# Performance work log

Measured on AMD Instinct MI355X. Metric: run time of the kernel, lower is better.

Reference implementation:

```python
import jax, jax.numpy as jnp
import numpy as np

V = 20000   # input_size (POI vocab)
U = 10000   # user_count
H = 128     # hidden_size
B = 64      # user_len (batch)
S = 200     # seq_len
LAM_T = 0.01
LAM_S = 100.0
DAY = 86400.0


def setup_inputs() -> dict:
    key = jax.random.key(0)
    ks = jax.random.split(key, 12)
    sc = 1.0 / np.sqrt(H)
    return {
        "poi_inputs": jax.random.randint(ks[0], (B, S), 0, V),
        "lengths": jnp.full((B,), S, dtype=jnp.int32),  # full sequences -> pack/pad is identity
        "timestamp_inputs": jnp.sort(jax.random.uniform(ks[1], (B, S), minval=0.0, maxval=DAY), axis=1),
        "location_inputs": jax.random.normal(ks[2], (B, S, 2)) * 0.1,
        "active_user": jax.random.randint(ks[3], (B,), 0, U),
        "emb_W": jax.random.normal(ks[4], (V, H)),      # nn.Embedding default N(0,1)
        "user_W": jax.random.normal(ks[5], (U, H)),
        "W_ih": jax.random.uniform(ks[6], (H, H), minval=-sc, maxval=sc),
        "W_hh": jax.random.uniform(ks[7], (H, H), minval=-sc, maxval=sc),
        "b_ih": jax.random.uniform(ks[8], (H,), minval=-sc, maxval=sc),
        "b_hh": jax.random.uniform(ks[9], (H,), minval=-sc, maxval=sc),
        "fc_W": jax.random.uniform(ks[10], (V, 2 * H), minval=-sc, maxval=sc),  # torch Linear [out,in]
        "fc_b": jax.random.uniform(ks[11], (V,), minval=-sc, maxval=sc),
    }


def _safe_norm(d):
    # norm over last axis with zero (not nan) gradient at d == 0
    d2 = jnp.sum(d * d, axis=-1)
    pos = d2 > 0
    return jnp.where(pos, jnp.sqrt(jnp.where(pos, d2, 1.0)), 0.0)


def reference(poi_inputs, lengths, timestamp_inputs, location_inputs, active_user,
              emb_W, user_W, W_ih, W_hh, b_ih, b_hh, fc_W, fc_b):
    t, s = timestamp_inputs, location_inputs
    x_emb = emb_W[poi_inputs]                       # [B,S,H]

    # vanilla tanh RNN (torch nn.RNN, batch_first) via scan over time
    def step(h, xt):
        h = jnp.tanh(xt @ W_ih.T + b_ih + h @ W_hh.T + b_hh)
        return h, h
    h0 = jnp.zeros((x_emb.shape[0], W_hh.shape[0]), x_emb.dtype)
    _, out = jax.lax.scan(step, h0, jnp.swapaxes(x_emb, 0, 1))
    out = jnp.swapaxes(out, 0, 1)                   # [B,S,H]

    # vectorized spatio-temporal decay attention (original O(S^2) python loop)
    dt = jnp.maximum(t[:, :, None] - t[:, None, :], 0.0)          # [B,S,S] clamp_min(0)
    ds = _safe_norm(s[:, :, None, :] - s[:, None, :, :])          # [B,S,S]
    a_j = ((jnp.cos(dt * (2.0 * jnp.pi / DAY)) + 1.0) * 0.5) * jnp.exp(-dt * LAM_T)
    b_j = jnp.exp(-ds * LAM_S)
    causal = jnp.tril(jnp.ones((t.shape[1], t.shape[1]), bool))   # j <= i
    w = jnp.where(causal, a_j * b_j + 1e-10, 0.0)                 # [B,S,S]
    sum_w = jnp.maximum(jnp.sum(w, axis=-1), 1e-10)               # [B,S]
    out_w = jnp.einsum('bij,bjh->bih', w, out) / sum_w[..., None] # [B,S,H]

    p_u = jnp.broadcast_to(user_W[active_user][:, None, :], out_w.shape)
    out_pu = jnp.concatenate([out_w, p_u], axis=-1)               # [B,S,2H]
    y = jax.nn.softmax(out_pu @ fc_W.T + fc_b, axis=-1)           # [B,S,V]
    return y, out_pu
```

## Files before the change

### kernel.cpp

```cpp
#include <hip/hip_runtime.h>
#include <hip/hip_bf16.h>
#include <stdint.h>

#define B_   64
#define S_   200
#define H_   128
#define V_   20000
#define M_   12800
#define NPAD 20224
#define NBN  158
#define NBM  100
#define NWG2 15800

#define WS_A      0u
#define WS_FCW    3276800u
#define WS_U      8454144u
#define WS_RSUM   13631488u
#define WS_WTIH   13682688u

#define XP_OFF    0
#define HOUT_OFF  2000000
#define PART_OFF  4000000
#define OUTPU_OFF 256000000ll

typedef __attribute__((ext_vector_type(8))) __bf16 bf16x8;
typedef __attribute__((ext_vector_type(4))) float  f32x4;

__device__ __forceinline__ void gll16(const void* g, void* l) {
  __builtin_amdgcn_global_load_lds(
      (const __attribute__((address_space(1))) void*)g,
      (__attribute__((address_space(3))) void*)l, 16, 0, 0);
}

__global__ __launch_bounds__(256)
void prep_w1(const float* __restrict__ fcw, __hip_bfloat16* __restrict__ w1) {
  int t = threadIdx.x;
  int row = blockIdx.x * 2 + (t >> 7);
  int col = t & 127;
  float v = (row < V_) ? fcw[(long)row * 256 + col] : 0.f;
  w1[(long)row * 128 + col] = __float2bfloat16(v);
}

__global__ __launch_bounds__(128)
void prep_wt(const float* __restrict__ w_ih, float* __restrict__ wt) {
  int bid = blockIdx.x, t = threadIdx.x;
  wt[bid * 128 + t] = w_ih[t * 128 + bid];
}

__global__ __launch_bounds__(256)
void user_k(const int* __restrict__ auser, const float* __restrict__ userW,
            const float* __restrict__ fcW, const float* __restrict__ fcb,
            float* __restrict__ U) {
  __shared__ float uw[8][128];
  int t = threadIdx.x;
  int c = blockIdx.x * 256 + t;
  int b0 = blockIdx.y * 8;
  for (int i = t; i < 8 * 128; i += 256) {
    int bb = i >> 7, kk = i & 127;
    uw[bb][kk] = userW[(long)auser[b0 + bb] * 128 + kk];
  }
  __syncthreads();
  float acc[8];
#pragma unroll
  for (int bb = 0; bb < 8; ++bb) acc[bb] = 0.f;
  if (c < V_) {
    const float* w2 = fcW + (long)c * 256 + 128;
#pragma unroll 4
    for (int k = 0; k < 128; k += 4) {
      float4 wv = *(const float4*)(w2 + k);
#pragma unroll
      for (int bb = 0; bb < 8; ++bb) {
        acc[bb] = fmaf(wv.x, uw[bb][k], acc[bb]);
        acc[bb] = fmaf(wv.y, uw[bb][k + 1], acc[bb]);
        acc[bb] = fmaf(wv.z, uw[bb][k + 2], acc[bb]);
        acc[bb] = fmaf(wv.w, uw[bb][k + 3], acc[bb]);
      }
    }
    float base = fcb[c];
#pragma unroll
    for (int bb = 0; bb < 8; ++bb)
      U[(long)(b0 + bb) * NPAD + c] = base + acc[bb];
  } else {
#pragma unroll
    for (int bb = 0; bb < 8; ++bb)
      U[(long)(b0 + bb) * NPAD + c] = -1e30f;
  }
}

__global__ __launch_bounds__(128)
void xproj_k(const int* __restrict__ poi, const float* __restrict__ emb,
             const float* __restrict__ wt_ih, const float* __restrict__ b_ih,
             const float* __restrict__ b_hh, float* __restrict__ xp) {
  __shared__ float xs[128];
  int m = blockIdx.x, j = threadIdx.x;
  xs[j] = emb[(long)poi[m] * 128 + j];
  __syncthreads();
  float acc = b_ih[j] + b_hh[j];
#pragma unroll 8
  for (int k = 0; k < 128; ++k) acc = fmaf(xs[k], wt_ih[k * 128 + j], acc);
  xp[(long)m * 128 + j] = acc;
}

__global__ __launch_bounds__(128)
void rnn_k(const float* __restrict__ xp, const float* __restrict__ w_hh,
           float* __restrict__ hout) {
  int b = blockIdx.x, j = threadIdx.x;
  float w[128];
#pragma unroll
  for (int k = 0; k < 128; ++k) w[k] = w_hh[j * 128 + k];
  __shared__ float hs[2][128];
  hs[0][j] = 0.f;
  __syncthreads();
  int cur = 0;
  for (int t = 0; t < S_; ++t) {
    float x0 = xp[((long)b * S_ + t) * 128 + j];
    const float* hp = hs[cur];
    float a0 = 0.f, a1 = 0.f, a2 = 0.f, a3 = 0.f;
#pragma unroll
    for (int k = 0; k < 32; ++k) {
      a0 = fmaf(hp[k],      w[k],      a0);
      a1 = fmaf(hp[k + 32], w[k + 32], a1);
      a2 = fmaf(hp[k + 64], w[k + 64], a2);
      a3 = fmaf(hp[k + 96], w[k + 96], a3);
    }
    float hn = tanhf(x0 + ((a0 + a1) + (a2 + a3)));
    hs[cur ^ 1][j] = hn;
    hout[((long)b * S_ + t) * 128 + j] = hn;
    cur ^= 1;
    __syncthreads();
  }
}

__global__ __launch_bounds__(128)
void attn_k(const float* __restrict__ ts, const float* __restrict__ loc,
            const float* __restrict__ hout, const int* __restrict__ auser,
            const float* __restrict__ userW, float* __restrict__ outpu,
            __hip_bfloat16* __restrict__ Abf) {
  int i = blockIdx.x, b = blockIdx.y, h = threadIdx.x;
  __shared__ float wl[128];
  const float OMEGA = 7.27220521664304e-05f;
  float ti = ts[b * S_ + i];
  float lx = loc[(b * S_ + i) * 2 + 0];
  float ly = loc[(b * S_ + i) * 2 + 1];
  float acc = 0.f, sw = 0.f;
  for (int jc = 0; jc <= i; jc += 128) {
    int j = jc + h;
    float wj = 0.f;
    if (j <= i) {
      float dt = fmaxf(ti - ts[b * S_ + j], 0.f);
      float a = (cosf(dt * OMEGA) + 1.f) * 0.5f * expf(-dt * 0.01f);
      float dx = lx - loc[(b * S_ + j) * 2 + 0];
      float dy = ly - loc[(b * S_ + j) * 2 + 1];
      float dn = sqrtf(dx * dx + dy * dy);
      wj = a * expf(-dn * 100.f) + 1e-10f;
    }
    __syncthreads();
    wl[h] = wj;
    __syncthreads();
    int lim = min(128, i - jc + 1);
    const float* hb = hout + ((long)b * S_ + jc) * 128 + h;
    for (int jj = 0; jj < lim; ++jj) {
      float wv = wl[jj];
      acc = fmaf(wv, hb[(long)jj * 128], acc);
      sw += wv;
    }
  }
  float ow = acc / fmaxf(sw, 1e-10f);
  long m = (long)b * S_ + i;
  float pu = userW[(long)auser[b] * 128 + h];
  outpu[m * 256 + h]       = ow;
  outpu[m * 256 + 128 + h] = pu;
  Abf[m * 128 + h]         = __float2bfloat16(ow);
}

template <int PASS>
__global__ __launch_bounds__(256)
void gemm_fc(const __hip_bfloat16* __restrict__ A,
             const __hip_bfloat16* __restrict__ Bw,
             const float* __restrict__ Ut,
             const float* __restrict__ rowsum,
             float* __restrict__ part,
             float* __restrict__ y) {
  __shared__ __align__(16) char smem[32768];
  __shared__ float rsum2[2][128];
  char* AsB = smem;
  char* BsB = smem + 8192;
  float* lbuf = (float*)smem;

  const int tid  = threadIdx.x;
  const int lane = tid & 63;
  const int wid  = tid >> 6;
  const int wr = wid >> 1, wc = wid & 1;
  const int g = lane >> 4, lr = lane & 15;

  const int orig = blockIdx.x;
  const int nid = (orig & 7) * (NWG2 / 8) + (orig >> 3);
  const int bn = nid / NBM, bm = nid % NBM;
  const long brow = (long)bm * 128, bcol = (long)bn * 128;

  f32x4 acc[4][4];
#pragma unroll
  for (int mi = 0; mi < 4; ++mi)
#pragma unroll
    for (int ni = 0; ni < 4; ++ni) acc[mi][ni] = (f32x4)(0.f);

  const char* Ab = (const char*)A + brow * 256;
  const char* Bb = (const char*)Bw + bcol * 256;
  const int c0 = tid, c1 = tid + 256;
  const int r0 = c0 >> 2, o0 = (c0 & 3) * 16;
  const int r1 = c1 >> 2, o1 = (c1 & 3) * 16;

  for (int kk = 0; kk < 4; ++kk) {
    __syncthreads();
    const int kb = kk * 64;
    gll16(Ab + (long)r0 * 256 + kb + o0, AsB + c0 * 16);
    gll16(Ab + (long)r1 * 256 + kb + o1, AsB + c1 * 16);
    gll16(Bb + (long)r0 * 256 + kb + o0, BsB + c0 * 16);
    gll16(Bb + (long)r1 * 256 + kb + o1, BsB + c1 * 16);
    __syncthreads();
    bf16x8 af[4], bfr[4];
#pragma unroll
    for (int mi = 0; mi < 4; ++mi)
      af[mi] = *(const bf16x8*)(AsB + (wr * 64 + mi * 16 + lr) * 64 + g * 16);
#pragma unroll
    for (int ni = 0; ni < 4; ++ni)
      bfr[ni] = *(const bf16x8*)(BsB + (wc * 64 + ni * 16 + lr) * 64 + g * 16);
#pragma unroll
    for (int mi = 0; mi < 4; ++mi)
#pragma unroll
      for (int ni = 0; ni < 4; ++ni)
        acc[mi][ni] = __builtin_amdgcn_mfma_f32_16x16x32_bf16(af[mi], bfr[ni], acc[mi][ni], 0, 0, 0);
  }

  if (PASS == 0) {
#pragma unroll
    for (int mi = 0; mi < 4; ++mi) {
#pragma unroll
      for (int r = 0; r < 4; ++r) {
        long row = brow + wr * 64 + mi * 16 + g * 4 + r;
        const float* urow = Ut + (long)(row / S_) * NPAD + bcol;
        float s = 0.f;
#pragma unroll
        for (int ni = 0; ni < 4; ++ni) {
          float u = urow[wc * 64 + ni * 16 + lr];
          s += __expf(acc[mi][ni][r] + u);
        }
#pragma unroll
        for (int off = 1; off < 16; off <<= 1) s += __shfl_xor(s, off);
        if (lr == 0) rsum2[wc][wr * 64 + mi * 16 + g * 4 + r] = s;
      }
    }
    __syncthreads();
    if (tid < 128)
      part[(long)bn * M_ + brow + tid] = rsum2[0][tid] + rsum2[1][tid];
  } else {
    if (bcol >= V_) return;
    const bool full = (bcol + 128 <= V_);
#pragma unroll
    for (int half = 0; half < 2; ++half) {
      __syncthreads();
      if (wr == half) {
#pragma unroll
        for (int mi = 0; mi < 4; ++mi) {
#pragma unroll
          for (int r = 0; r < 4; ++r) {
            int lrow = mi * 16 + g * 4 + r;
            long row = brow + half * 64 + lrow;
            const float* urow = Ut + (long)(row / S_) * NPAD + bcol;
            float inv = 1.0f / rowsum[row];
#pragma unroll
            for (int ni = 0; ni < 4; ++ni) {
              int lcol = wc * 64 + ni * 16 + lr;
              lbuf[lrow * 128 + lcol] = __expf(acc[mi][ni][r] + urow[lcol]) * inv;
            }
          }
        }
      }
      __syncthreads();
      if (full) {
#pragma unroll
        for (int it = 0; it < 8; ++it) {
          int idx = it * 256 + tid;
          int lrow = idx >> 5, c4 = idx & 31;
          long row = brow + half * 64 + lrow;
          *(float4*)(y + row * (long)V_ + bcol + c4 * 4) = ((const float4*)lbuf)[idx];
        }
      } else {
#pragma unroll
        for (int it = 0; it < 8; ++it) {
          int idx = it * 256 + tid;
          int lrow = idx >> 5, c4 = idx & 31;
          long row = brow + half * 64 + lrow;
#pragma unroll
          for (int e = 0; e < 4; ++e) {
            int col = (int)bcol + c4 * 4 + e;
            if (col < V_) y[row * (long)V_ + col] = lbuf[lrow * 128 + c4 * 4 + e];
          }
        }
      }
    }
  }
}

__global__ void reduce_rows(const float* __restrict__ part, float* __restrict__ rowsum) {
  int m = blockIdx.x * 256 + threadIdx.x;
  if (m < M_) {
    float s = 0.f;
    for (int bn = 0; bn < NBN; ++bn) s += part[(long)bn * M_ + m];
    rowsum[m] = fmaxf(s, 1e-30f);
  }
}

extern "C" void kernel_launch(void* const* d_in, const int* in_sizes, int n_in,
                              void* d_out, int out_size, void* d_ws, size_t ws_size,
                              hipStream_t stream) {
  const int*   poi   = (const int*)d_in[0];
  const float* ts    = (const float*)d_in[2];
  const float* loc   = (const float*)d_in[3];
  const int*   auser = (const int*)d_in[4];
  const float* embW  = (const float*)d_in[5];
  const float* userW = (const float*)d_in[6];
  const float* w_ih  = (const float*)d_in[7];
  const float* w_hh  = (const float*)d_in[8];
  const float* b_ih  = (const float*)d_in[9];
  const float* b_hh  = (const float*)d_in[10];
  const float* fcW   = (const float*)d_in[11];
  const float* fcb   = (const float*)d_in[12];

  float* out = (float*)d_out;
  char*  ws  = (char*)d_ws;
  __hip_bfloat16* Abf    = (__hip_bfloat16*)(ws + WS_A);
  __hip_bfloat16* w1b    = (__hip_bfloat16*)(ws + WS_FCW);
  float*          Ut     = (float*)(ws + WS_U);
  float*          rowsum = (float*)(ws + WS_RSUM);
  float*          wt_ih  = (float*)(ws + WS_WTIH);

  float* xp    = out + XP_OFF;
  float* hout  = out + HOUT_OFF;
  float* part  = out + PART_OFF;
  float* outpu = out + OUTPU_OFF;

  prep_w1<<<dim3(NPAD / 2), dim3(256), 0, stream>>>(fcW, w1b);
  prep_wt<<<dim3(128), dim3(128), 0, stream>>>(w_ih, wt_ih);
  user_k<<<dim3(NPAD / 256, 8), dim3(256), 0, stream>>>(auser, userW, fcW, fcb, Ut);
  xproj_k<<<dim3(M_), dim3(128), 0, stream>>>(poi, embW, wt_ih, b_ih, b_hh, xp);
  rnn_k<<<dim3(B_), dim3(128), 0, stream>>>(xp, w_hh, hout);
  attn_k<<<dim3(S_, B_), dim3(128), 0, stream>>>(ts, loc, hout, auser, userW, outpu, Abf);
  gemm_fc<0><<<dim3(NWG2), dim3(256), 0, stream>>>(Abf, w1b, Ut, nullptr, part, nullptr);
  reduce_rows<<<dim3(50), dim3(256), 0, stream>>>(part, rowsum);
  gemm_fc<1><<<dim3(NWG2), dim3(256), 0, stream>>>(Abf, w1b, Ut, rowsum, nullptr, out);
}
```

Baseline: 828.2 us.

## Enlarge FC GEMM tiles to 256x256 with full-K LDS staging and XOR swizzle

The two-pass FC softmax GEMM now uses 256x256 output tiles with 512 threads. The whole K=128 slice of A and B is loaded into 128KB of LDS in one go, with an XOR swizzle to avoid bank conflicts, and the per-K synchronisations are dropped. The XCD block remap now handles a block count that is not a multiple of 8. The aim is to cut redundant global reads of A and fcW and to reduce barrier overhead. In exchange, LDS use and register pressure rise (acc grows to 8x4), which limits occupancy to one block per CU.

```diff
diff --git a/kernel.cpp b/kernel.cpp
--- a/kernel.cpp
+++ b/kernel.cpp
@@ -8,9 +8,9 @@
 #define V_   20000
 #define M_   12800
 #define NPAD 20224
-#define NBN  158
-#define NBM  100
-#define NWG2 15800
+#define NBN  79
+#define NBM  50
+#define NWG  3950
 
 #define WS_A      0u
 #define WS_FCW    3276800u
@@ -174,59 +174,69 @@
 }
 
 template <int PASS>
-__global__ __launch_bounds__(256)
+__global__ __launch_bounds__(512)
 void gemm_fc(const __hip_bfloat16* __restrict__ A,
              const __hip_bfloat16* __restrict__ Bw,
              const float* __restrict__ Ut,
              const float* __restrict__ rowsum,
              float* __restrict__ part,
              float* __restrict__ y) {
-  __shared__ __align__(16) char smem[32768];
-  __shared__ float rsum2[2][128];
+  __shared__ __align__(16) char smem[131072];
+  __shared__ float rsum4[4][256];
   char* AsB = smem;
-  char* BsB = smem + 8192;
+  char* BsB = smem + 65536;
   float* lbuf = (float*)smem;
 
   const int tid  = threadIdx.x;
   const int lane = tid & 63;
   const int wid  = tid >> 6;
-  const int wr = wid >> 1, wc = wid & 1;
+  const int wr = wid >> 2, wc = wid & 3;
   const int g = lane >> 4, lr = lane & 15;
 
   const int orig = blockIdx.x;
-  const int nid = (orig & 7) * (NWG2 / 8) + (orig >> 3);
+  const int qq = NWG >> 3, rr = NWG & 7;
+  const int xcd = orig & 7, lix = orig >> 3;
+  const int nid = (xcd < rr ? xcd * (qq + 1) : rr * (qq + 1) + (xcd - rr) * qq) + lix;
   const int bn = nid / NBM, bm = nid % NBM;
-  const long brow = (long)bm * 128, bcol = (long)bn * 128;
-
-  f32x4 acc[4][4];
-#pragma unroll
-  for (int mi = 0; mi < 4; ++mi)
-#pragma unroll
-    for (int ni = 0; ni < 4; ++ni) acc[mi][ni] = (f32x4)(0.f);
+  const long brow = (long)bm * 256, bcol = (long)bn * 256;
 
   const char* Ab = (const char*)A + brow * 256;
   const char* Bb = (const char*)Bw + bcol * 256;
-  const int c0 = tid, c1 = tid + 256;
-  const int r0 = c0 >> 2, o0 = (c0 & 3) * 16;
-  const int r1 = c1 >> 2, o1 = (c1 & 3) * 16;
-
+
+#pragma unroll
+  for (int i = 0; i < 8; ++i) {
+    int ci = i * 512 + tid;
+    int row = ci >> 4;
+    int w = (ci & 15) ^ (row & 7);
+    long src = (long)row * 256 + (long)w * 16;
+    gll16(Ab + src, AsB + (long)ci * 16);
+    gll16(Bb + src, BsB + (long)ci * 16);
+  }
+  __syncthreads();
+
+  f32x4 acc[8][4];
+#pragma unroll
+  for (int mi = 0; mi < 8; ++mi)
+#pragma unroll
+    for (int ni = 0; ni < 4; ++ni) acc[mi][ni] = (f32x4)(0.f);
+
+#pragma unroll
   for (int kk = 0; kk < 4; ++kk) {
-    __syncthreads();
-    const int kb = kk * 64;
-    gll16(Ab + (long)r0 * 256 + kb + o0, AsB + c0 * 16);
-    gll16(Ab + (long)r1 * 256 + kb + o1, AsB + c1 * 16);
-    gll16(Bb + (long)r0 * 256 + kb + o0, BsB + c0 * 16);
-    gll16(Bb + (long)r1 * 256 + kb + o1, BsB + c1 * 16);
-    __syncthreads();
-    bf16x8 af[4], bfr[4];
-#pragma unroll
-    for (int mi = 0; mi < 4; ++mi)
-      af[mi] = *(const bf16x8*)(AsB + (wr * 64 + mi * 16 + lr) * 64 + g * 16);
-#pragma unroll
-    for (int ni = 0; ni < 4; ++ni)
-      bfr[ni] = *(const bf16x8*)(BsB + (wc * 64 + ni * 16 + lr) * 64 + g * 16);
-#pragma unroll
-    for (int mi = 0; mi < 4; ++mi)
+    bf16x8 af[8], bfr[4];
+#pragma unroll
+    for (int mi = 0; mi < 8; ++mi) {
+      int row = wr * 128 + mi * 16 + lr;
+      int w = ((kk << 2) | g) ^ (row & 7);
+      af[mi] = *(const bf16x8*)(AsB + row * 256 + w * 16);
+    }
+#pragma unroll
+    for (int ni = 0; ni < 4; ++ni) {
+      int row = wc * 64 + ni * 16 + lr;
+      int w = ((kk << 2) | g) ^ (row & 7);
+      bfr[ni] = *(const bf16x8*)(BsB + row * 256 + w * 16);
+    }
+#pragma unroll
+    for (int mi = 0; mi < 8; ++mi)
 #pragma unroll
       for (int ni = 0; ni < 4; ++ni)
         acc[mi][ni] = __builtin_amdgcn_mfma_f32_16x16x32_bf16(af[mi], bfr[ni], acc[mi][ni], 0, 0, 0);
@@ -234,10 +244,10 @@
 
   if (PASS == 0) {
 #pragma unroll
-    for (int mi = 0; mi < 4; ++mi) {
+    for (int mi = 0; mi < 8; ++mi) {
 #pragma unroll
       for (int r = 0; r < 4; ++r) {
-        long row = brow + wr * 64 + mi * 16 + g * 4 + r;
+        long row = brow + wr * 128 + mi * 16 + g * 4 + r;
         const float* urow = Ut + (long)(row / S_) * NPAD + bcol;
         float s = 0.f;
 #pragma unroll
@@ -247,31 +257,31 @@
         }
 #pragma unroll
         for (int off = 1; off < 16; off <<= 1) s += __shfl_xor(s, off);
-        if (lr == 0) rsum2[wc][wr * 64 + mi * 16 + g * 4 + r] = s;
+        if (lr == 0) rsum4[wc][wr * 128 + mi * 16 + g * 4 + r] = s;
       }
     }
     __syncthreads();
-    if (tid < 128)
-      part[(long)bn * M_ + brow + tid] = rsum2[0][tid] + rsum2[1][tid];
+    if (tid < 256)
+      part[(long)bn * M_ + brow + tid] =
+          rsum4[0][tid] + rsum4[1][tid] + rsum4[2][tid] + rsum4[3][tid];
   } else {
-    if (bcol >= V_) return;
-    const bool full = (bcol + 128 <= V_);
+    const bool full = (bcol + 256 <= V_);
 #pragma unroll
     for (int half = 0; half < 2; ++half) {
       __syncthreads();
       if (wr == half) {
 #pragma unroll
-        for (int mi = 0; mi < 4; ++mi) {
+        for (int mi = 0; mi < 8; ++mi) {
 #pragma unroll
           for (int r = 0; r < 4; ++r) {
             int lrow = mi * 16 + g * 4 + r;
-            long row = brow + half * 64 + lrow;
+            long row = brow + half * 128 + lrow;
             const float* urow = Ut + (long)(row / S_) * NPAD + bcol;
             float inv = 1.0f / rowsum[row];
 #pragma unroll
             for (int ni = 0; ni < 4; ++ni) {
               int lcol = wc * 64 + ni * 16 + lr;
-              lbuf[lrow * 128 + lcol] = __expf(acc[mi][ni][r] + urow[lcol]) * inv;
+              lbuf[lrow * 256 + lcol] = __expf(acc[mi][ni][r] + urow[lcol]) * inv;
             }
           }
         }
@@ -279,22 +289,22 @@
       __syncthreads();
       if (full) {
 #pragma unroll
-        for (int it = 0; it < 8; ++it) {
-          int idx = it * 256 + tid;
-          int lrow = idx >> 5, c4 = idx & 31;
-          long row = brow + half * 64 + lrow;
+        for (int it = 0; it < 16; ++it) {
+          int idx = it * 512 + tid;
+          int lrow = idx >> 6, c4 = idx & 63;
+          long row = brow + half * 128 + lrow;
           *(float4*)(y + row * (long)V_ + bcol + c4 * 4) = ((const float4*)lbuf)[idx];
         }
       } else {
 #pragma unroll
-        for (int it = 0; it < 8; ++it) {
-          int idx = it * 256 + tid;
-          int lrow = idx >> 5, c4 = idx & 31;
-          long row = brow + half * 64 + lrow;
+        for (int it = 0; it < 16; ++it) {
+          int idx = it * 512 + tid;
+          int lrow = idx >> 6, c4 = idx & 63;
+          long row = brow + half * 128 + lrow;
 #pragma unroll
           for (int e = 0; e < 4; ++e) {
             int col = (int)bcol + c4 * 4 + e;
-            if (col < V_) y[row * (long)V_ + col] = lbuf[lrow * 128 + c4 * 4 + e];
+            if (col < V_) y[row * (long)V_ + col] = lbuf[lrow * 256 + c4 * 4 + e];
           }
         }
       }
@@ -346,7 +356,7 @@
   xproj_k<<<dim3(M_), dim3(128), 0, stream>>>(poi, embW, wt_ih, b_ih, b_hh, xp);
   rnn_k<<<dim3(B_), dim3(128), 0, stream>>>(xp, w_hh, hout);
   attn_k<<<dim3(S_, B_), dim3(128), 0, stream>>>(ts, loc, hout, auser, userW, outpu, Abf);
-  gemm_fc<0><<<dim3(NWG2), dim3(256), 0, stream>>>(Abf, w1b, Ut, nullptr, part, nullptr);
+  gemm_fc<0><<<dim3(NWG), dim3(512), 0, stream>>>(Abf, w1b, Ut, nullptr, part, nullptr);
   reduce_rows<<<dim3(50), dim3(256), 0, stream>>>(part, rowsum);
-  gemm_fc<1><<<dim3(NWG2), dim3(256), 0, stream>>>(Abf, w1b, Ut, rowsum, nullptr, out);
-}
+  gemm_fc<1><<<dim3(NWG), dim3(512), 0, stream>>>(Abf, w1b, Ut, rowsum, nullptr, out);
+}
```

Result: faster. 807.3 us (-2.5%).
